# Optimization experiments

Measured on AMD Instinct MI355X. Metric: run time of the kernel, lower is better.

## Reference

```python
import jax, jax.numpy as jnp
import numpy as np

B, S, E, H = 2, 2048, 1024, 16
D = E // H  # head dim = 64

def setup_inputs() -> dict:
    key = jax.random.key(0)
    ks = jax.random.split(key, 7)
    mk = lambda k, shape, scale=1.0: (jax.random.normal(k, shape, dtype=jnp.float32) * scale)
    return {
        "query": mk(ks[0], (B, S, E)),
        "key": mk(ks[1], (B, S, E)),
        "value": mk(ks[2], (B, S, E)),
        "Wq": mk(ks[3], (E, E), 1.0 / np.sqrt(E)),
        "Wk": mk(ks[4], (E, E), 1.0 / np.sqrt(E)),
        "Wv": mk(ks[5], (E, E), 1.0 / np.sqrt(E)),
        "Wo": mk(ks[6], (E, E), 1.0 / np.sqrt(E)),
    }

def reference(query, key, value, Wq, Wk, Wv, Wo):
    # nn.Linear(bias=False): y = x @ W.T
    def split_heads(x):
        return x.reshape(B, -1, H, D).transpose(0, 2, 1, 3)  # [B,H,S,D]
    q = split_heads(query @ Wq.T)
    k = split_heads(key @ Wk.T)
    v = split_heads(value @ Wv.T)
    scores = jnp.einsum("bhqd,bhkd->bhqk", q, k) / jnp.sqrt(jnp.float32(D))
    attn = jax.nn.softmax(scores, axis=-1)  # dropout p=0 -> identity
    out = jnp.einsum("bhqk,bhkd->bhqd", attn, v)
    out = out.transpose(0, 2, 1, 3).reshape(B, -1, E)
    out = out @ Wo.T
    return out
```

## Files before the change

### kernel.cpp

```cpp
#include <hip/hip_runtime.h>
#include <stdint.h>

#define S_LEN 2048
#define HDIM  64
#define EMB   1024
#define NTOK  4096

typedef short bf16x8 __attribute__((ext_vector_type(8)));
typedef float f32x4  __attribute__((ext_vector_type(4)));

__device__ __forceinline__ unsigned short f32_bf16(float f) {
  union { float f; uint32_t u; } v; v.f = f;
  return (unsigned short)((v.u + 0x7fffu + ((v.u >> 16) & 1u)) >> 16);
}

__device__ __forceinline__ uint32_t fbits(float f) {
  union { float f; uint32_t u; } v; v.f = f; return v.u;
}

__device__ __forceinline__ uint32_t pack_bf16_trunc(float lo, float hi) {
  return __builtin_amdgcn_perm(fbits(hi), fbits(lo), 0x07060302u);
}

__device__ __forceinline__ uint32_t pack_bf16_rne(float lo, float hi) {
  return (uint32_t)f32_bf16(lo) | ((uint32_t)f32_bf16(hi) << 16);
}

__device__ __forceinline__ void async_ld16(const unsigned short* g, unsigned short* l) {
  __builtin_amdgcn_global_load_lds(
      (__attribute__((address_space(1))) unsigned int*)(uintptr_t)g,
      (__attribute__((address_space(3))) unsigned int*)l, 16, 0, 0);
}

#define CL2 0.18033688f

__global__ void cast_all(const float* __restrict__ q, const float* __restrict__ k,
                         const float* __restrict__ v, const float* __restrict__ Wq,
                         const float* __restrict__ Wk, const float* __restrict__ Wv,
                         const float* __restrict__ Wo,
                         unsigned short* __restrict__ qb, unsigned short* __restrict__ kb,
                         unsigned short* __restrict__ vb, unsigned short* __restrict__ wqb,
                         unsigned short* __restrict__ wkb, unsigned short* __restrict__ wvb,
                         unsigned short* __restrict__ wob) {
  const int b = blockIdx.x;
  const float* src; unsigned short* dst; int base;
  float scl = 1.0f;
  if (b < 12288) {
    const int which = b >> 12; base = b & 4095;
    src = which == 0 ? q : which == 1 ? k : v;
    dst = which == 0 ? qb : which == 1 ? kb : vb;
  } else {
    const int bb = b - 12288, which = bb >> 10; base = bb & 1023;
    src = which == 0 ? Wq : which == 1 ? Wk : which == 2 ? Wv : Wo;
    dst = which == 0 ? wqb : which == 1 ? wkb : which == 2 ? wvb : wob;
    if (which == 0) scl = CL2;
  }
  const int i = base * 256 + threadIdx.x;
  float4 f = ((const float4*)src)[i];
  ushort4 o;
  o.x = f32_bf16(f.x * scl); o.y = f32_bf16(f.y * scl);
  o.z = f32_bf16(f.z * scl); o.w = f32_bf16(f.w * scl);
  ((ushort4*)dst)[i] = o;
}

__global__ __launch_bounds__(256)
void gemm_qkv(const unsigned short* __restrict__ qb, const unsigned short* __restrict__ kb,
              const unsigned short* __restrict__ vb, const unsigned short* __restrict__ wqb,
              const unsigned short* __restrict__ wkb, const unsigned short* __restrict__ wvb,
              unsigned short* __restrict__ Qh, unsigned short* __restrict__ Kh,
              unsigned short* __restrict__ Vt) {
  __shared__ __align__(16) unsigned short As[2 * 128 * 32];
  __shared__ __align__(16) unsigned short Bs[2 * 128 * 32];

  const int z  = blockIdx.z;
  const int bx = blockIdx.y;
  const int by = blockIdx.x;
  const unsigned short* Xp = z == 0 ? qb  : z == 1 ? kb  : vb;
  const unsigned short* Wp = z == 0 ? wqb : z == 1 ? wkb : wvb;

  const unsigned short *A, *B;
  int tileM, tileN;
  if (z < 2) { A = Wp; tileM = bx * 128; B = Xp; tileN = by * 128; }
  else       { A = Xp; tileM = by * 128; B = Wp; tileN = bx * 128; }

  const int tid  = threadIdx.x;
  const int lane = tid & 63;
  const int wave = tid >> 6;
  const int wm = (wave >> 1) * 64;
  const int wn = (wave & 1) * 64;
  const int ccol = lane & 15;
  const int cgrp = lane >> 4;
  const int rchunk = lane >> 2;
  const int coff   = (lane & 3) * 8;

  f32x4 acc[4][4];
#pragma unroll
  for (int i = 0; i < 4; ++i)
#pragma unroll
    for (int j = 0; j < 4; ++j) acc[i][j] = 0.f;

  for (int k0 = 0; k0 < EMB; k0 += 64) {
#pragma unroll
    for (int kk = 0; kk < 2; ++kk)
#pragma unroll
      for (int i = 0; i < 2; ++i) {
        const int c = wave * 2 + i;
        const int row = c * 16 + rchunk;
        async_ld16(A + (size_t)(tileM + row) * EMB + k0 + kk * 32 + coff,
                   As + kk * 4096 + c * 512);
        async_ld16(B + (size_t)(tileN + row) * EMB + k0 + kk * 32 + coff,
                   Bs + kk * 4096 + c * 512);
      }
    __syncthreads();
#pragma unroll
    for (int kk = 0; kk < 2; ++kk) {
      bf16x8 af[4], bfm[4];
#pragma unroll
      for (int i = 0; i < 4; ++i) {
        af[i]  = *(const bf16x8*)(As + kk * 4096 + (wm + i * 16 + ccol) * 32 + cgrp * 8);
        bfm[i] = *(const bf16x8*)(Bs + kk * 4096 + (wn + i * 16 + ccol) * 32 + cgrp * 8);
      }
#pragma unroll
      for (int i = 0; i < 4; ++i)
#pragma unroll
        for (int j = 0; j < 4; ++j)
          acc[i][j] = __builtin_amdgcn_mfma_f32_16x16x32_bf16(af[i], bfm[j], acc[i][j], 0, 0, 0);
    }
    __syncthreads();
  }

  if (z < 2) {
    unsigned short* Oh = (z == 0) ? Qh : Kh;
#pragma unroll
    for (int i = 0; i < 4; ++i) {
      const int gd = tileM + wm + i * 16 + cgrp * 4;
      const int h = gd >> 6, dd = gd & 63;
#pragma unroll
      for (int j = 0; j < 4; ++j) {
        const int gt = tileN + wn + j * 16 + ccol;
        const int b = gt >> 11, s = gt & 2047;
        const uint32_t u0 = pack_bf16_rne(acc[i][j][0], acc[i][j][1]);
        const uint32_t u1 = pack_bf16_rne(acc[i][j][2], acc[i][j][3]);
        *(int2*)&Oh[((size_t)((b * 16 + h) * 2048 + s)) * 64 + dd] =
            make_int2((int)u0, (int)u1);
      }
    }
  } else {
#pragma unroll
    for (int i = 0; i < 4; ++i) {
      const int gt = tileM + wm + i * 16 + cgrp * 4;
      const int b = gt >> 11, s = gt & 2047;
#pragma unroll
      for (int j = 0; j < 4; ++j) {
        const int gd = tileN + wn + j * 16 + ccol;
        const int h = gd >> 6, dd = gd & 63;
        const uint32_t u0 = pack_bf16_rne(acc[i][j][0], acc[i][j][1]);
        const uint32_t u1 = pack_bf16_rne(acc[i][j][2], acc[i][j][3]);
        *(int2*)&Vt[((size_t)((b * 16 + h) * 64 + dd)) * 2048 + s] =
            make_int2((int)u0, (int)u1);
      }
    }
  }
}

__global__ __launch_bounds__(256)
void gemm_out(const unsigned short* __restrict__ Ctx, const unsigned short* __restrict__ Wo,
              float* __restrict__ Out) {
  __shared__ __align__(16) unsigned short As[2 * 64 * 32];
  __shared__ __align__(16) unsigned short Bs[2 * 128 * 32];

  const int tid  = threadIdx.x;
  const int lane = tid & 63;
  const int wave = tid >> 6;
  const int wm = (wave >> 1) * 32;
  const int wn = (wave & 1) * 64;
  const int ccol = lane & 15;
  const int cgrp = lane >> 4;
  const int rchunk = lane >> 2;
  const int coff   = (lane & 3) * 8;
  const int tileM = blockIdx.y * 64;
  const int tileN = blockIdx.x * 128;

  f32x4 acc[2][4];
#pragma unroll
  for (int i = 0; i < 2; ++i)
#pragma unroll
    for (int j = 0; j < 4; ++j) acc[i][j] = 0.f;

  for (int k0 = 0; k0 < EMB; k0 += 64) {
#pragma unroll
    for (int kk = 0; kk < 2; ++kk) {
      {
        const int row = wave * 16 + rchunk;
        async_ld16(Wo + (size_t)(tileM + row) * EMB + k0 + kk * 32 + coff,
                   As + kk * 2048 + wave * 512);
      }
#pragma unroll
      for (int i = 0; i < 2; ++i) {
        const int c = wave * 2 + i;
        const int row = c * 16 + rchunk;
        async_ld16(Ctx + (size_t)(tileN + row) * EMB + k0 + kk * 32 + coff,
                   Bs + kk * 4096 + c * 512);
      }
    }
    __syncthreads();
#pragma unroll
    for (int kk = 0; kk < 2; ++kk) {
      bf16x8 af[2], bfm[4];
#pragma unroll
      for (int i = 0; i < 2; ++i)
        af[i] = *(const bf16x8*)(As + kk * 2048 + (wm + i * 16 + ccol) * 32 + cgrp * 8);
#pragma unroll
      for (int j = 0; j < 4; ++j)
        bfm[j] = *(const bf16x8*)(Bs + kk * 4096 + (wn + j * 16 + ccol) * 32 + cgrp * 8);
#pragma unroll
      for (int i = 0; i < 2; ++i)
#pragma unroll
        for (int j = 0; j < 4; ++j)
          acc[i][j] = __builtin_amdgcn_mfma_f32_16x16x32_bf16(af[i], bfm[j], acc[i][j], 0, 0, 0);
    }
    __syncthreads();
  }

#pragma unroll
  for (int i = 0; i < 2; ++i) {
    const int odim = tileM + wm + i * 16 + cgrp * 4;
#pragma unroll
    for (int j = 0; j < 4; ++j) {
      const int gt = tileN + wn + j * 16 + ccol;
      float4 o = make_float4(acc[i][j][0], acc[i][j][1], acc[i][j][2], acc[i][j][3]);
      *(float4*)&Out[(size_t)gt * 1024 + odim] = o;
    }
  }
}

__global__ __launch_bounds__(256, 4)
void attn_kernel(const unsigned short* __restrict__ Qh,
                 const unsigned short* __restrict__ Kh,
                 const unsigned short* __restrict__ Vt,
                 unsigned short* __restrict__ Ctx) {
  __shared__ __align__(16) unsigned short Ks[2 * 64 * 64];
  __shared__ __align__(16) unsigned short Vs[2 * 64 * 64];
  __shared__ __align__(16) unsigned short Ps[4 * 16 * 64];

  const int tid  = threadIdx.x;
  const int lane = tid & 63;
  const int wave = tid >> 6;
  const int bh = blockIdx.x;
  const int q0 = blockIdx.y * 64;
  const unsigned short* Qg = Qh + ((size_t)bh * S_LEN + q0) * HDIM;
  const unsigned short* Kg = Kh + (size_t)bh * S_LEN * HDIM;
  const unsigned short* Vg = Vt + (size_t)bh * HDIM * S_LEN;

  const int ccol = lane & 15;
  const int cgrp = lane >> 4;
  const int mrow = wave * 16;
  const int sw7  = ccol & 7;

#pragma unroll
  for (int i = 0; i < 2; ++i) {
    const int cid = i * 256 + tid;
    const int row = cid >> 3, j = cid & 7, g = j ^ (row & 7);
    *(int4*)&Ps[row * 64 + j * 8] = *(const int4*)&Qg[(size_t)row * 64 + g * 8];
  }
  __syncthreads();
  bf16x8 aq[2];
#pragma unroll
  for (int kk = 0; kk < 2; ++kk) {
    const int pp = (kk * 4 + cgrp) ^ sw7;
    aq[kk] = *(const bf16x8*)&Ps[(mrow + ccol) * 64 + pp * 8];
  }
  unsigned short* Pw = Ps + wave * 1024;

  const int r0 = tid >> 3, j0 = tid & 7;
  const int r1 = r0 + 32;
  const int sA = j0 ^ (r0 & 7);
  const int sB = j0 ^ (r1 & 7);

  int4 kr0 = *(const int4*)&Kg[(size_t)r0 * 64 + sA * 8];
  int4 kr1 = *(const int4*)&Kg[(size_t)r1 * 64 + sB * 8];
  int4 vr0 = *(const int4*)&Vg[(size_t)r0 * 2048 + sA * 8];
  int4 vr1 = *(const int4*)&Vg[(size_t)r1 * 2048 + sB * 8];

  f32x4 l4 = 0.f;
  f32x4 o_acc[4];
#pragma unroll
  for (int dt = 0; dt < 4; ++dt) o_acc[dt] = 0.f;

  for (int i = 0; i < 32; ++i) {
    unsigned short* Kb = Ks + (i & 1) * 4096;
    unsigned short* Vb = Vs + (i & 1) * 4096;
    *(int4*)&Kb[r0 * 64 + j0 * 8] = kr0;
    *(int4*)&Kb[r1 * 64 + j0 * 8] = kr1;
    *(int4*)&Vb[r0 * 64 + j0 * 8] = vr0;
    *(int4*)&Vb[r1 * 64 + j0 * 8] = vr1;
    __syncthreads();
    if (i < 31) {
      const int nb = (i + 1) * 64;
      kr0 = *(const int4*)&Kg[(size_t)(nb + r0) * 64 + sA * 8];
      kr1 = *(const int4*)&Kg[(size_t)(nb + r1) * 64 + sB * 8];
      vr0 = *(const int4*)&Vg[(size_t)r0 * 2048 + nb + sA * 8];
      vr1 = *(const int4*)&Vg[(size_t)r1 * 2048 + nb + sB * 8];
    }

    f32x4 sc[4];
#pragma unroll
    for (int nt = 0; nt < 4; ++nt) {
      f32x4 s = 0.f;
#pragma unroll
      for (int kk = 0; kk < 2; ++kk) {
        const int krow = nt * 16 + ccol;
        const int c8 = (kk * 4 + cgrp) ^ (krow & 7);
        bf16x8 ak = *(const bf16x8*)&Kb[krow * 64 + c8 * 8];
        s = __builtin_amdgcn_mfma_f32_16x16x32_bf16(ak, aq[kk], s, 0, 0, 0);
      }
      sc[nt] = s;
    }

#pragma unroll
    for (int nt = 0; nt < 4; ++nt) {
#pragma unroll
      for (int r = 0; r < 4; ++r)
        sc[nt][r] = __builtin_amdgcn_exp2f(sc[nt][r]);
      l4 += sc[nt];
    }

#pragma unroll
    for (int nt = 0; nt < 4; ++nt) {
      const uint32_t u0 = pack_bf16_trunc(sc[nt][0], sc[nt][1]);
      const uint32_t u1 = pack_bf16_trunc(sc[nt][2], sc[nt][3]);
      const int pp = (nt * 2 + (cgrp >> 1)) ^ sw7;
      *(int2*)&Pw[ccol * 64 + pp * 8 + (cgrp & 1) * 4] = make_int2((int)u0, (int)u1);
    }
    asm volatile("s_waitcnt lgkmcnt(0)" ::: "memory");
    bf16x8 ap[2];
#pragma unroll
    for (int kk = 0; kk < 2; ++kk) {
      const int pp = (kk * 4 + cgrp) ^ sw7;
      ap[kk] = *(const bf16x8*)&Pw[ccol * 64 + pp * 8];
    }

#pragma unroll
    for (int dt = 0; dt < 4; ++dt) {
      f32x4 o = o_acc[dt];
#pragma unroll
      for (int kk = 0; kk < 2; ++kk) {
        const int vrow = dt * 16 + ccol;
        const int c8 = (kk * 4 + cgrp) ^ (vrow & 7);
        bf16x8 av = *(const bf16x8*)&Vb[vrow * 64 + c8 * 8];
        o = __builtin_amdgcn_mfma_f32_16x16x32_bf16(av, ap[kk], o, 0, 0, 0);
      }
      o_acc[dt] = o;
    }
  }

  float l_i = l4[0] + l4[1] + l4[2] + l4[3];
  l_i += __shfl_xor(l_i, 16);
  l_i += __shfl_xor(l_i, 32);
  const int b = bh >> 4, h = bh & 15;
  const float inv_l = __builtin_amdgcn_rcpf(l_i) * 1.00195f;
  const int srow = q0 + mrow + ccol;
#pragma unroll
  for (int dt = 0; dt < 4; ++dt) {
    float o0 = o_acc[dt][0] * inv_l, o1 = o_acc[dt][1] * inv_l;
    float o2 = o_acc[dt][2] * inv_l, o3 = o_acc[dt][3] * inv_l;
    uint32_t u0 = pack_bf16_rne(o0, o1);
    uint32_t u1 = pack_bf16_rne(o2, o3);
    const int col = h * 64 + dt * 16 + cgrp * 4;
    *(int2*)&Ctx[((size_t)(b * 2048 + srow)) * 1024 + col] = make_int2((int)u0, (int)u1);
  }
}

extern "C" void kernel_launch(void* const* d_in, const int* in_sizes, int n_in,
                              void* d_out, int out_size, void* d_ws, size_t ws_size,
                              hipStream_t stream) {
  const float* q  = (const float*)d_in[0];
  const float* k  = (const float*)d_in[1];
  const float* v  = (const float*)d_in[2];
  const float* Wq = (const float*)d_in[3];
  const float* Wk = (const float*)d_in[4];
  const float* Wv = (const float*)d_in[5];
  const float* Wo = (const float*)d_in[6];

  const size_t tok = (size_t)NTOK * EMB;
  const size_t wsz = (size_t)EMB * EMB;
  unsigned short* p = (unsigned short*)d_ws;
  unsigned short* qb  = p; p += tok;
  unsigned short* kb  = p; p += tok;
  unsigned short* vb  = p; p += tok;
  unsigned short* wqb = p; p += wsz;
  unsigned short* wkb = p; p += wsz;
  unsigned short* wvb = p; p += wsz;
  unsigned short* wob = p; p += wsz;
  unsigned short* Qh  = p; p += tok;
  unsigned short* Kh  = p; p += tok;
  unsigned short* Vt  = p; p += tok;
  unsigned short* Ctx = p; p += tok;

  cast_all<<<dim3(16384), dim3(256), 0, stream>>>(q, k, v, Wq, Wk, Wv, Wo,
                                                  qb, kb, vb, wqb, wkb, wvb, wob);

  gemm_qkv<<<dim3(32, 8, 3), dim3(256), 0, stream>>>(qb, kb, vb, wqb, wkb, wvb,
                                                     Qh, Kh, Vt);

  attn_kernel<<<dim3(32, 32), dim3(256), 0, stream>>>(Qh, Kh, Vt, Ctx);

  gemm_out<<<dim3(32, 16), dim3(256), 0, stream>>>(Ctx, wob, (float*)d_out);
}
```

Baseline: 218.7 us.

## Process 128 query rows per attention block, two 16-row groups per wave

The attention kernel now handles 128 query rows per block instead of 64, with each wave computing two 16-row query groups. Each K and V fragment read from LDS feeds two MFMAs, which halves LDS reads and global K/V traffic per query row. The cost is more registers for the doubled accumulators (occupancy bound lowered to 2), a larger P buffer in LDS, and half as many blocks (512), which may leave CUs less evenly loaded.

```diff
diff --git a/kernel.cpp b/kernel.cpp
--- a/kernel.cpp
+++ b/kernel.cpp
@@ -234,43 +234,45 @@
   }
 }
 
-__global__ __launch_bounds__(256, 4)
+__global__ __launch_bounds__(256, 2)
 void attn_kernel(const unsigned short* __restrict__ Qh,
                  const unsigned short* __restrict__ Kh,
                  const unsigned short* __restrict__ Vt,
                  unsigned short* __restrict__ Ctx) {
   __shared__ __align__(16) unsigned short Ks[2 * 64 * 64];
   __shared__ __align__(16) unsigned short Vs[2 * 64 * 64];
-  __shared__ __align__(16) unsigned short Ps[4 * 16 * 64];
+  __shared__ __align__(16) unsigned short Ps[128 * 64];
 
   const int tid  = threadIdx.x;
   const int lane = tid & 63;
   const int wave = tid >> 6;
   const int bh = blockIdx.x;
-  const int q0 = blockIdx.y * 64;
+  const int q0 = blockIdx.y * 128;
   const unsigned short* Qg = Qh + ((size_t)bh * S_LEN + q0) * HDIM;
   const unsigned short* Kg = Kh + (size_t)bh * S_LEN * HDIM;
   const unsigned short* Vg = Vt + (size_t)bh * HDIM * S_LEN;
 
   const int ccol = lane & 15;
   const int cgrp = lane >> 4;
-  const int mrow = wave * 16;
+  const int mrow = wave * 32;
   const int sw7  = ccol & 7;
 
 #pragma unroll
-  for (int i = 0; i < 2; ++i) {
+  for (int i = 0; i < 4; ++i) {
     const int cid = i * 256 + tid;
     const int row = cid >> 3, j = cid & 7, g = j ^ (row & 7);
     *(int4*)&Ps[row * 64 + j * 8] = *(const int4*)&Qg[(size_t)row * 64 + g * 8];
   }
   __syncthreads();
-  bf16x8 aq[2];
-#pragma unroll
-  for (int kk = 0; kk < 2; ++kk) {
-    const int pp = (kk * 4 + cgrp) ^ sw7;
-    aq[kk] = *(const bf16x8*)&Ps[(mrow + ccol) * 64 + pp * 8];
-  }
-  unsigned short* Pw = Ps + wave * 1024;
+  bf16x8 aq[2][2];
+#pragma unroll
+  for (int g = 0; g < 2; ++g)
+#pragma unroll
+    for (int kk = 0; kk < 2; ++kk) {
+      const int pp = (kk * 4 + cgrp) ^ sw7;
+      aq[g][kk] = *(const bf16x8*)&Ps[(mrow + g * 16 + ccol) * 64 + pp * 8];
+    }
+  unsigned short* Pw = Ps + wave * 2048;
 
   const int r0 = tid >> 3, j0 = tid & 7;
   const int r1 = r0 + 32;
@@ -282,10 +284,11 @@
   int4 vr0 = *(const int4*)&Vg[(size_t)r0 * 2048 + sA * 8];
   int4 vr1 = *(const int4*)&Vg[(size_t)r1 * 2048 + sB * 8];
 
-  f32x4 l4 = 0.f;
-  f32x4 o_acc[4];
-#pragma unroll
-  for (int dt = 0; dt < 4; ++dt) o_acc[dt] = 0.f;
+  f32x4 l4[2];
+  l4[0] = 0.f; l4[1] = 0.f;
+  f32x4 o_acc[4][2];
+#pragma unroll
+  for (int dt = 0; dt < 4; ++dt) { o_acc[dt][0] = 0.f; o_acc[dt][1] = 0.f; }
 
   for (int i = 0; i < 32; ++i) {
     unsigned short* Kb = Ks + (i & 1) * 4096;
@@ -303,71 +306,84 @@
       vr1 = *(const int4*)&Vg[(size_t)r1 * 2048 + nb + sB * 8];
     }
 
-    f32x4 sc[4];
+    f32x4 sc[2][4];
 #pragma unroll
     for (int nt = 0; nt < 4; ++nt) {
-      f32x4 s = 0.f;
+      const int krow = nt * 16 + ccol;
+      bf16x8 ak0 = *(const bf16x8*)&Kb[krow * 64 + ((cgrp) ^ sw7) * 8];
+      bf16x8 ak1 = *(const bf16x8*)&Kb[krow * 64 + ((4 + cgrp) ^ sw7) * 8];
+#pragma unroll
+      for (int g = 0; g < 2; ++g) {
+        f32x4 s = 0.f;
+        s = __builtin_amdgcn_mfma_f32_16x16x32_bf16(ak0, aq[g][0], s, 0, 0, 0);
+        s = __builtin_amdgcn_mfma_f32_16x16x32_bf16(ak1, aq[g][1], s, 0, 0, 0);
+        sc[g][nt] = s;
+      }
+    }
+
+#pragma unroll
+    for (int g = 0; g < 2; ++g)
+#pragma unroll
+      for (int nt = 0; nt < 4; ++nt) {
+#pragma unroll
+        for (int r = 0; r < 4; ++r)
+          sc[g][nt][r] = __builtin_amdgcn_exp2f(sc[g][nt][r]);
+        l4[g] += sc[g][nt];
+      }
+
+#pragma unroll
+    for (int g = 0; g < 2; ++g) {
+      unsigned short* Pr = Pw + (g * 16 + ccol) * 64;
+#pragma unroll
+      for (int nt = 0; nt < 4; ++nt) {
+        const uint32_t u0 = pack_bf16_trunc(sc[g][nt][0], sc[g][nt][1]);
+        const uint32_t u1 = pack_bf16_trunc(sc[g][nt][2], sc[g][nt][3]);
+        const int pp = (nt * 2 + (cgrp >> 1)) ^ sw7;
+        *(int2*)&Pr[pp * 8 + (cgrp & 1) * 4] = make_int2((int)u0, (int)u1);
+      }
+    }
+    asm volatile("s_waitcnt lgkmcnt(0)" ::: "memory");
+    bf16x8 ap[2][2];
+#pragma unroll
+    for (int g = 0; g < 2; ++g)
 #pragma unroll
       for (int kk = 0; kk < 2; ++kk) {
-        const int krow = nt * 16 + ccol;
-        const int c8 = (kk * 4 + cgrp) ^ (krow & 7);
-        bf16x8 ak = *(const bf16x8*)&Kb[krow * 64 + c8 * 8];
-        s = __builtin_amdgcn_mfma_f32_16x16x32_bf16(ak, aq[kk], s, 0, 0, 0);
-      }
-      sc[nt] = s;
-    }
-
-#pragma unroll
-    for (int nt = 0; nt < 4; ++nt) {
-#pragma unroll
-      for (int r = 0; r < 4; ++r)
-        sc[nt][r] = __builtin_amdgcn_exp2f(sc[nt][r]);
-      l4 += sc[nt];
-    }
-
-#pragma unroll
-    for (int nt = 0; nt < 4; ++nt) {
-      const uint32_t u0 = pack_bf16_trunc(sc[nt][0], sc[nt][1]);
-      const uint32_t u1 = pack_bf16_trunc(sc[nt][2], sc[nt][3]);
-      const int pp = (nt * 2 + (cgrp >> 1)) ^ sw7;
-      *(int2*)&Pw[ccol * 64 + pp * 8 + (cgrp & 1) * 4] = make_int2((int)u0, (int)u1);
-    }
-    asm volatile("s_waitcnt lgkmcnt(0)" ::: "memory");
-    bf16x8 ap[2];
-#pragma unroll
-    for (int kk = 0; kk < 2; ++kk) {
-      const int pp = (kk * 4 + cgrp) ^ sw7;
-      ap[kk] = *(const bf16x8*)&Pw[ccol * 64 + pp * 8];
-    }
+        const int pp = (kk * 4 + cgrp) ^ sw7;
+        ap[g][kk] = *(const bf16x8*)&Pw[(g * 16 + ccol) * 64 + pp * 8];
+      }
 
 #pragma unroll
     for (int dt = 0; dt < 4; ++dt) {
-      f32x4 o = o_acc[dt];
-#pragma unroll
-      for (int kk = 0; kk < 2; ++kk) {
-        const int vrow = dt * 16 + ccol;
-        const int c8 = (kk * 4 + cgrp) ^ (vrow & 7);
-        bf16x8 av = *(const bf16x8*)&Vb[vrow * 64 + c8 * 8];
-        o = __builtin_amdgcn_mfma_f32_16x16x32_bf16(av, ap[kk], o, 0, 0, 0);
-      }
-      o_acc[dt] = o;
-    }
-  }
-
-  float l_i = l4[0] + l4[1] + l4[2] + l4[3];
-  l_i += __shfl_xor(l_i, 16);
-  l_i += __shfl_xor(l_i, 32);
+      const int vrow = dt * 16 + ccol;
+      bf16x8 av0 = *(const bf16x8*)&Vb[vrow * 64 + ((cgrp) ^ sw7) * 8];
+      bf16x8 av1 = *(const bf16x8*)&Vb[vrow * 64 + ((4 + cgrp) ^ sw7) * 8];
+#pragma unroll
+      for (int g = 0; g < 2; ++g) {
+        f32x4 o = o_acc[dt][g];
+        o = __builtin_amdgcn_mfma_f32_16x16x32_bf16(av0, ap[g][0], o, 0, 0, 0);
+        o = __builtin_amdgcn_mfma_f32_16x16x32_bf16(av1, ap[g][1], o, 0, 0, 0);
+        o_acc[dt][g] = o;
+      }
+    }
+  }
+
   const int b = bh >> 4, h = bh & 15;
-  const float inv_l = __builtin_amdgcn_rcpf(l_i) * 1.00195f;
-  const int srow = q0 + mrow + ccol;
-#pragma unroll
-  for (int dt = 0; dt < 4; ++dt) {
-    float o0 = o_acc[dt][0] * inv_l, o1 = o_acc[dt][1] * inv_l;
-    float o2 = o_acc[dt][2] * inv_l, o3 = o_acc[dt][3] * inv_l;
-    uint32_t u0 = pack_bf16_rne(o0, o1);
-    uint32_t u1 = pack_bf16_rne(o2, o3);
-    const int col = h * 64 + dt * 16 + cgrp * 4;
-    *(int2*)&Ctx[((size_t)(b * 2048 + srow)) * 1024 + col] = make_int2((int)u0, (int)u1);
+#pragma unroll
+  for (int g = 0; g < 2; ++g) {
+    float l_i = l4[g][0] + l4[g][1] + l4[g][2] + l4[g][3];
+    l_i += __shfl_xor(l_i, 16);
+    l_i += __shfl_xor(l_i, 32);
+    const float inv_l = __builtin_amdgcn_rcpf(l_i) * 1.00195f;
+    const int srow = q0 + mrow + g * 16 + ccol;
+#pragma unroll
+    for (int dt = 0; dt < 4; ++dt) {
+      float o0 = o_acc[dt][g][0] * inv_l, o1 = o_acc[dt][g][1] * inv_l;
+      float o2 = o_acc[dt][g][2] * inv_l, o3 = o_acc[dt][g][3] * inv_l;
+      uint32_t u0 = pack_bf16_rne(o0, o1);
+      uint32_t u1 = pack_bf16_rne(o2, o3);
+      const int col = h * 64 + dt * 16 + cgrp * 4;
+      *(int2*)&Ctx[((size_t)(b * 2048 + srow)) * 1024 + col] = make_int2((int)u0, (int)u1);
+    }
   }
 }
 
@@ -403,7 +419,7 @@
   gemm_qkv<<<dim3(32, 8, 3), dim3(256), 0, stream>>>(qb, kb, vb, wqb, wkb, wvb,
                                                      Qh, Kh, Vt);
 
-  attn_kernel<<<dim3(32, 32), dim3(256), 0, stream>>>(Qh, Kh, Vt, Ctx);
+  attn_kernel<<<dim3(32, 16), dim3(256), 0, stream>>>(Qh, Kh, Vt, Ctx);
 
   gemm_out<<<dim3(32, 16), dim3(256), 0, stream>>>(Ctx, wob, (float*)d_out);
 }
```

After: 214.1 us. -2.1%, faster.
